# Performance work log

Measured on AMD Instinct MI355X. Metric: run time of the kernel, lower is better.

## Reference

```python
import jax, jax.numpy as jnp
import numpy as np

N_NODES = 100000
N_EDGES = 1600000


def setup_inputs() -> dict:
    key = jax.random.key(0)
    k1, k2, k3, k4 = jax.random.split(key, 4)
    in_c, hid_c, out_c = 128, 128, 64
    x = jax.random.normal(k1, (N_NODES, in_c), dtype=jnp.float32)
    edge_index = jax.random.randint(k2, (2, N_EDGES), 0, N_NODES, dtype=jnp.int64)
    W1 = jax.random.normal(k3, (in_c, hid_c), dtype=jnp.float32) * (1.0 / np.sqrt(in_c))
    b1 = jnp.zeros((hid_c,), dtype=jnp.float32)
    W2 = jax.random.normal(k4, (hid_c, out_c), dtype=jnp.float32) * (1.0 / np.sqrt(hid_c))
    b2 = jnp.zeros((out_c,), dtype=jnp.float32)
    return {"x": x, "edge_index": edge_index, "W1": W1, "b1": b1, "W2": W2, "b2": b2}


def reference(x, edge_index, W1, b1, W2, b2):
    # PyG GCNConv default: add self-loops, symmetric deg normalization, bias.
    N = x.shape[0]
    loops = jnp.arange(N, dtype=edge_index.dtype)
    src = jnp.concatenate([edge_index[0], loops])  # message sources (j)
    dst = jnp.concatenate([edge_index[1], loops])  # aggregation targets (i)
    ones = jnp.ones(src.shape[0], dtype=x.dtype)
    deg = jax.ops.segment_sum(ones, dst, num_segments=N)  # in-degree incl. self-loops
    dis = jnp.where(deg > 0, jax.lax.rsqrt(deg), 0.0)     # deg^{-1/2}, inf->0
    norm = dis[src] * dis[dst]                             # [E+N]

    def gcn(h, W, b):
        h = h @ W                                  # linear transform first (fewer bytes moved)
        msg = h[src] * norm[:, None]               # gather + scale, [E+N, C]
        return jax.ops.segment_sum(msg, dst, num_segments=N) + b

    h = jax.nn.relu(gcn(x, W1, b1))
    return gcn(h, W2, b2)
```

## Files before the change

kernel.cpp:

```cpp
#include <hip/hip_runtime.h>


constexpr int SCAN_CHUNK = 4096;
constexpr int NBKT = 512;
constexpr int EPB  = 8192;
constexpr int CSR_CAP = 12288;

using short8 = __attribute__((ext_vector_type(8))) short;
using f32x4  = __attribute__((ext_vector_type(4))) float;

__device__ __forceinline__ unsigned short f2bf(float f) {
  unsigned u = __float_as_uint(f);
  unsigned r = (u + 0x7FFFu + ((u >> 16) & 1u)) >> 16;
  return (unsigned short)r;
}
__device__ __forceinline__ float bf2f(unsigned short h) {
  return __uint_as_float(((unsigned)h) << 16);
}

__device__ __forceinline__ int ld_idx(const void* ei, int is64, long long i) {
  return is64 ? (int)((const long long*)ei)[i] : ((const int*)ei)[i];
}

__device__ __forceinline__ int sniff64(const unsigned* ei, int tid) {
  unsigned v = (tid < 128) ? ei[2 * tid + 1] : 0u;
  return __syncthreads_or((int)(v != 0u)) ? 0 : 1;
}


__global__ __launch_bounds__(256) void ks_part_g(const int* __restrict__ in,
                                                 int* __restrict__ partial, int m) {
  __shared__ int red[256];
  int b = blockIdx.x, tid = threadIdx.x;
  int base = b * SCAN_CHUNK + tid * 16;
  int s = 0;
#pragma unroll
  for (int i = 0; i < 16; ++i) {
    int idx = base + i;
    if (idx < m) s += in[idx];
  }
  red[tid] = s;
  __syncthreads();
  for (int off = 128; off > 0; off >>= 1) {
    if (tid < off) red[tid] += red[tid + off];
    __syncthreads();
  }
  if (tid == 0) partial[b] = red[0];
}

__global__ __launch_bounds__(256) void k_scan_top(int* __restrict__ partial, int nparts) {
  __shared__ int sums[256];
  int tid = threadIdx.x;
  sums[tid] = (tid < nparts) ? partial[tid] : 0;
  __syncthreads();
  for (int off = 1; off < 256; off <<= 1) {
    int t = (tid >= off) ? sums[tid - off] : 0;
    __syncthreads();
    sums[tid] += t;
    __syncthreads();
  }
  if (tid < nparts) partial[tid] = (tid == 0) ? 0 : sums[tid - 1];
}

__global__ __launch_bounds__(256) void ks_write_g(const int* __restrict__ in,
                                                  const int* __restrict__ partial,
                                                  int* __restrict__ out, int m) {
  __shared__ int tsum[256];
  int b = blockIdx.x, tid = threadIdx.x;
  int base = b * SCAN_CHUNK + tid * 16;
  int vals[16];
  int s = 0;
#pragma unroll
  for (int i = 0; i < 16; ++i) {
    int idx = base + i;
    int v = (idx < m) ? in[idx] : 0;
    vals[i] = s;
    s += v;
  }
  tsum[tid] = s;
  __syncthreads();
  for (int off = 1; off < 256; off <<= 1) {
    int t = (tid >= off) ? tsum[tid - off] : 0;
    __syncthreads();
    tsum[tid] += t;
    __syncthreads();
  }
  int toff = partial[b] + ((tid == 0) ? 0 : tsum[tid - 1]);
#pragma unroll
  for (int i = 0; i < 16; ++i) {
    int idx = base + i;
    if (idx < m) out[idx] = toff + vals[i];
  }
}


__global__ __launch_bounds__(256) void k_hist(const void* __restrict__ ei,
                                              int* __restrict__ hist,
                                              int e, int nblk, int npb) {
  __shared__ int h[NBKT];
  int blk = blockIdx.x, tid = threadIdx.x;
  int is64 = sniff64((const unsigned*)ei, tid);
  for (int i = tid; i < NBKT; i += 256) h[i] = 0;
  __syncthreads();
  int base = blk * EPB;
  int end = base + EPB; if (end > e) end = e;
  for (int i = base + tid; i < end; i += 256) {
    int d = ld_idx(ei, is64, (long long)e + i);
    atomicAdd(&h[d / npb], 1);
  }
  __syncthreads();
  for (int i = tid; i < NBKT; i += 256)
    hist[(size_t)i * nblk + blk] = h[i];
}

__global__ __launch_bounds__(256) void k_partition(const void* __restrict__ ei,
                                                   const int* __restrict__ scanned,
                                                   unsigned* __restrict__ pairbuf,
                                                   int e, int nblk, int npb) {
  __shared__ int off[NBKT];
  int blk = blockIdx.x, tid = threadIdx.x;
  int is64 = sniff64((const unsigned*)ei, tid);
  for (int i = tid; i < NBKT; i += 256)
    off[i] = scanned[(size_t)i * nblk + blk];
  __syncthreads();
  int base = blk * EPB;
  int end = base + EPB; if (end > e) end = e;
  for (int i = base + tid; i < end; i += 256) {
    int s = ld_idx(ei, is64, i);
    int d = ld_idx(ei, is64, (long long)e + i);
    int bkt = d / npb;
    int pos = atomicAdd(&off[bkt], 1);
    pairbuf[pos] = (unsigned)s | ((unsigned)(d - bkt * npb) << 20);
  }
}

__global__ __launch_bounds__(256) void k_bucket_all(const unsigned* __restrict__ pairbuf,
                                                    const int* __restrict__ scanned,
                                                    int* __restrict__ rowptr,
                                                    int* __restrict__ cursor,
                                                    float* __restrict__ dis,
                                                    int* __restrict__ csr,
                                                    int n, int e, int npb, int nblk) {
  __shared__ int lcsr[CSR_CAP];
  __shared__ int cnt[256];
  __shared__ int scn[256];
  int b = blockIdx.x, tid = threadIdx.x;
  if (b == 0 && tid == 0) rowptr[n] = e;
  int lo = b * npb;
  if (lo >= n) return;
  int hi = lo + npb; if (hi > n) hi = n;
  int nn = hi - lo;
  int seg_base = scanned[(size_t)b * nblk];
  int seg_end  = (b == NBKT - 1) ? e : scanned[(size_t)(b + 1) * nblk];
  int cnt_total = seg_end - seg_base;

  for (int i = tid; i < nn; i += 256) cnt[i] = 0;
  __syncthreads();
  for (int i = tid; i < cnt_total; i += 256)
    atomicAdd(&cnt[pairbuf[seg_base + i] >> 20], 1);
  __syncthreads();

  int v = (tid < nn) ? cnt[tid] : 0;
  scn[tid] = v;
  __syncthreads();
  for (int off = 1; off < 256; off <<= 1) {
    int t = (tid >= off) ? scn[tid - off] : 0;
    __syncthreads();
    scn[tid] += t;
    __syncthreads();
  }
  int start = (tid == 0) ? 0 : scn[tid - 1];
  if (tid < nn) {
    int node = lo + tid;
    rowptr[node] = seg_base + start;
    cursor[node] = seg_base + start;
    dis[node] = rsqrtf((float)(v + 1));
  }
  __syncthreads();
  if (tid < nn) cnt[tid] = start;
  __syncthreads();

  if (cnt_total <= CSR_CAP) {
    for (int i = tid; i < cnt_total; i += 256) {
      unsigned p = pairbuf[seg_base + i];
      int q = atomicAdd(&cnt[p >> 20], 1);
      lcsr[q] = (int)(p & 0xFFFFFu);
    }
    __syncthreads();
    for (int i = tid; i < cnt_total; i += 256) csr[seg_base + i] = lcsr[i];
  } else {
    for (int i = tid; i < cnt_total; i += 256) {
      unsigned p = pairbuf[seg_base + i];
      int q = atomicAdd(&cursor[lo + (int)(p >> 20)], 1);
      csr[q] = (int)(p & 0xFFFFFu);
    }
  }
}

template <int NCOL, bool XBF16>
__global__ __launch_bounds__(256) void k_gemm_mfma(const void* __restrict__ Xv,
                                                   const float* __restrict__ W,
                                                   const float* __restrict__ dis,
                                                   unsigned short* __restrict__ S,
                                                   int nrows) {
  constexpr int ROWS = 64;
  constexpr int NCF = NCOL / 16;
  __shared__ __align__(16) unsigned short xs[ROWS * 128];
  __shared__ __align__(16) unsigned short wt[NCOL * 128];
  int tid = threadIdx.x;

  for (int id = tid; id < 128 * NCOL; id += 256) {
    int k = id / NCOL, c = id % NCOL;
    wt[(c * 128 + k) ^ ((c & 7) << 3)] = f2bf(W[id]);
  }

  int wv = tid >> 6, lane = tid & 63;
  int l16 = lane & 15, lk = lane >> 4;
  int arow = wv * 16 + l16;
  int npass = (nrows + ROWS - 1) / ROWS;

  for (int p = blockIdx.x; p < npass; p += gridDim.x) {
    int r0 = p * ROWS;
    __syncthreads();
#pragma unroll
    for (int it = 0; it < 4; ++it) {
      int id = tid + 256 * it;
      int row = id >> 4, kc = id & 15;
      int gr = r0 + row;
      unsigned short v[8];
      if (gr < nrows) {
        if (XBF16) {
          const unsigned short* xb = (const unsigned short*)Xv + (size_t)gr * 128 + kc * 8;
#pragma unroll
          for (int j = 0; j < 8; ++j) v[j] = xb[j];
        } else {
          const float4* x4 = (const float4*)Xv + (size_t)gr * 32 + kc * 2;
          float4 f0 = x4[0], f1 = x4[1];
          v[0] = f2bf(f0.x); v[1] = f2bf(f0.y); v[2] = f2bf(f0.z); v[3] = f2bf(f0.w);
          v[4] = f2bf(f1.x); v[5] = f2bf(f1.y); v[6] = f2bf(f1.z); v[7] = f2bf(f1.w);
        }
      } else {
#pragma unroll
        for (int j = 0; j < 8; ++j) v[j] = 0;
      }
      int idx = (row * 128 + kc * 8) ^ ((row & 7) << 3);
      *(short8*)&xs[idx] = *(short8*)v;
    }
    __syncthreads();

    short8 a[4];
#pragma unroll
    for (int ks = 0; ks < 4; ++ks)
      a[ks] = *(short8*)&xs[(arow * 128 + ks * 32 + lk * 8) ^ ((arow & 7) << 3)];

    f32x4 acc[NCF];
#pragma unroll
    for (int cf = 0; cf < NCF; ++cf) acc[cf] = (f32x4){0.f, 0.f, 0.f, 0.f};

#pragma unroll
    for (int cf = 0; cf < NCF; ++cf) {
      int col = cf * 16 + l16;
#pragma unroll
      for (int ks = 0; ks < 4; ++ks) {
        short8 bfr = *(short8*)&wt[(col * 128 + ks * 32 + lk * 8) ^ ((col & 7) << 3)];
        acc[cf] = __builtin_amdgcn_mfma_f32_16x16x32_bf16(a[ks], bfr, acc[cf], 0, 0, 0);
      }
    }

#pragma unroll
    for (int r = 0; r < 4; ++r) {
      int gr = r0 + wv * 16 + lk * 4 + r;
      if (gr < nrows) {
        float dv = dis[gr];
#pragma unroll
        for (int cf = 0; cf < NCF; ++cf)
          S[(size_t)gr * NCOL + cf * 16 + l16] = f2bf(acc[cf][r] * dv);
      }
    }
  }
}

__global__ __launch_bounds__(256) void k_agg1(const unsigned short* __restrict__ S,
                                              const int* __restrict__ rowptr,
                                              const int* __restrict__ csr,
                                              const float* __restrict__ dis,
                                              const float* __restrict__ b1,
                                              unsigned short* __restrict__ H, int n) {
  int node = blockIdx.x * 4 + (threadIdx.x >> 6);
  if (node >= n) return;
  int lane = threadIdx.x & 63;
  int eg = lane >> 4;
  int cp = lane & 15;
  float acc[8];
  if (eg == 0) {
    short8 v = *(const short8*)&S[(size_t)node * 128 + cp * 8];
#pragma unroll
    for (int k = 0; k < 8; ++k) acc[k] = bf2f((unsigned short)v[k]);
  } else {
#pragma unroll
    for (int k = 0; k < 8; ++k) acc[k] = 0.f;
  }
  int2 rp = *(const int2*)&rowptr[node];
  int e = rp.x + eg;
  for (; e + 12 < rp.y; e += 16) {
    int j0 = csr[e], j1 = csr[e + 4], j2 = csr[e + 8], j3 = csr[e + 12];
    short8 v0 = *(const short8*)&S[(size_t)j0 * 128 + cp * 8];
    short8 v1 = *(const short8*)&S[(size_t)j1 * 128 + cp * 8];
    short8 v2 = *(const short8*)&S[(size_t)j2 * 128 + cp * 8];
    short8 v3 = *(const short8*)&S[(size_t)j3 * 128 + cp * 8];
#pragma unroll
    for (int k = 0; k < 8; ++k)
      acc[k] += (bf2f((unsigned short)v0[k]) + bf2f((unsigned short)v1[k])) +
                (bf2f((unsigned short)v2[k]) + bf2f((unsigned short)v3[k]));
  }
  for (; e < rp.y; e += 4) {
    int j = csr[e];
    short8 v = *(const short8*)&S[(size_t)j * 128 + cp * 8];
#pragma unroll
    for (int k = 0; k < 8; ++k) acc[k] += bf2f((unsigned short)v[k]);
  }
#pragma unroll
  for (int k = 0; k < 8; ++k) {
    acc[k] += __shfl_xor(acc[k], 16);
    acc[k] += __shfl_xor(acc[k], 32);
  }
  if (eg == 0) {
    float d = dis[node];
    float4 bb0 = ((const float4*)b1)[cp * 2];
    float4 bb1 = ((const float4*)b1)[cp * 2 + 1];
    float bv[8] = {bb0.x, bb0.y, bb0.z, bb0.w, bb1.x, bb1.y, bb1.z, bb1.w};
    short8 o;
#pragma unroll
    for (int k = 0; k < 8; ++k)
      o[k] = (short)f2bf(fmaxf(fmaf(acc[k], d, bv[k]), 0.f));
    *(short8*)&H[(size_t)node * 128 + cp * 8] = o;
  }
}

__global__ __launch_bounds__(256) void k_agg2(const unsigned short* __restrict__ S,
                                              const int* __restrict__ rowptr,
                                              const int* __restrict__ csr,
                                              const float* __restrict__ dis,
                                              const float* __restrict__ b2,
                                              float* __restrict__ O, int n) {
  int node = blockIdx.x * 4 + (threadIdx.x >> 6);
  if (node >= n) return;
  int lane = threadIdx.x & 63;
  int eg = lane >> 3;
  int cp = lane & 7;
  float acc[8];
  if (eg == 0) {
    short8 v = *(const short8*)&S[(size_t)node * 64 + cp * 8];
#pragma unroll
    for (int k = 0; k < 8; ++k) acc[k] = bf2f((unsigned short)v[k]);
  } else {
#pragma unroll
    for (int k = 0; k < 8; ++k) acc[k] = 0.f;
  }
  int2 rp = *(const int2*)&rowptr[node];
  int e = rp.x + eg;
  for (; e + 24 < rp.y; e += 32) {
    int j0 = csr[e], j1 = csr[e + 8], j2 = csr[e + 16], j3 = csr[e + 24];
    short8 v0 = *(const short8*)&S[(size_t)j0 * 64 + cp * 8];
    short8 v1 = *(const short8*)&S[(size_t)j1 * 64 + cp * 8];
    short8 v2 = *(const short8*)&S[(size_t)j2 * 64 + cp * 8];
    short8 v3 = *(const short8*)&S[(size_t)j3 * 64 + cp * 8];
#pragma unroll
    for (int k = 0; k < 8; ++k)
      acc[k] += (bf2f((unsigned short)v0[k]) + bf2f((unsigned short)v1[k])) +
                (bf2f((unsigned short)v2[k]) + bf2f((unsigned short)v3[k]));
  }
  for (; e < rp.y; e += 8) {
    int j = csr[e];
    short8 v = *(const short8*)&S[(size_t)j * 64 + cp * 8];
#pragma unroll
    for (int k = 0; k < 8; ++k) acc[k] += bf2f((unsigned short)v[k]);
  }
#pragma unroll
  for (int k = 0; k < 8; ++k) {
    acc[k] += __shfl_xor(acc[k], 8);
    acc[k] += __shfl_xor(acc[k], 16);
    acc[k] += __shfl_xor(acc[k], 32);
  }
  if (eg == 0) {
    float d = dis[node];
    float4 bb0 = ((const float4*)b2)[cp * 2];
    float4 bb1 = ((const float4*)b2)[cp * 2 + 1];
    float bv[8] = {bb0.x, bb0.y, bb0.z, bb0.w, bb1.x, bb1.y, bb1.z, bb1.w};
    float4 o0, o1;
    o0.x = fmaf(acc[0], d, bv[0]); o0.y = fmaf(acc[1], d, bv[1]);
    o0.z = fmaf(acc[2], d, bv[2]); o0.w = fmaf(acc[3], d, bv[3]);
    o1.x = fmaf(acc[4], d, bv[4]); o1.y = fmaf(acc[5], d, bv[5]);
    o1.z = fmaf(acc[6], d, bv[6]); o1.w = fmaf(acc[7], d, bv[7]);
    ((float4*)O)[(size_t)node * 16 + cp * 2] = o0;
    ((float4*)O)[(size_t)node * 16 + cp * 2 + 1] = o1;
  }
}

extern "C" void kernel_launch(void* const* d_in, const int* in_sizes, int n_in,
                              void* d_out, int out_size, void* d_ws, size_t ws_size,
                              hipStream_t stream) {
  const float* x  = (const float*)d_in[0];
  const void*  ei = d_in[1];
  const float* W1 = (const float*)d_in[2];
  const float* b1 = (const float*)d_in[3];
  const float* W2 = (const float*)d_in[4];
  const float* b2 = (const float*)d_in[5];
  float* out = (float*)d_out;

  const int N = in_sizes[0] / 128;
  const int E = in_sizes[1] / 2;
  const int npb  = (N + NBKT - 1) / NBKT;
  const int nblk = (E + EPB - 1) / EPB;
  const int m    = NBKT * nblk;

  char* w = (char*)d_ws;
  size_t off = 0;
  auto alloc = [&](size_t bytes) -> void* {
    void* p = (void*)(w + off);
    off += (bytes + 255) & ~(size_t)255;
    return p;
  };
  int*            rowptr  = (int*)alloc((size_t)(N + 1) * 4);
  int*            cursor  = (int*)alloc((size_t)N * 4);
  float*          dis     = (float*)alloc((size_t)N * 4);
  int*            csr     = (int*)alloc((size_t)E * 4);
  unsigned*       pairbuf = (unsigned*)alloc((size_t)E * 4);
  int*            hist    = (int*)alloc((size_t)m * 4);
  int*            scanned = (int*)alloc((size_t)m * 4);
  unsigned short* s1      = (unsigned short*)alloc((size_t)N * 128 * 2);
  unsigned short* s2      = (unsigned short*)alloc((size_t)N * 64 * 2);
  unsigned short* h       = (unsigned short*)alloc((size_t)N * 128 * 2);
  int*            partial = (int*)alloc(256 * 4);

  int npartsM = (m + SCAN_CHUNK - 1) / SCAN_CHUNK;

  k_hist<<<nblk, 256, 0, stream>>>(ei, hist, E, nblk, npb);
  ks_part_g<<<npartsM, 256, 0, stream>>>(hist, partial, m);
  k_scan_top<<<1, 256, 0, stream>>>(partial, npartsM);
  ks_write_g<<<npartsM, 256, 0, stream>>>(hist, partial, scanned, m);
  k_partition<<<nblk, 256, 0, stream>>>(ei, scanned, pairbuf, E, nblk, npb);
  k_bucket_all<<<NBKT, 256, 0, stream>>>(pairbuf, scanned, rowptr, cursor, dis, csr,
                                         N, E, npb, nblk);

  k_gemm_mfma<128, false><<<1024, 256, 0, stream>>>(x, W1, dis, s1, N);
  k_agg1<<<(N + 3) / 4, 256, 0, stream>>>(s1, rowptr, csr, dis, b1, h, N);
  k_gemm_mfma<64, true><<<1024, 256, 0, stream>>>(h, W2, dis, s2, N);
  k_agg2<<<(N + 3) / 4, 256, 0, stream>>>(s2, rowptr, csr, dis, b2, out, N);
}
```

Baseline: 214.9 us.

## Shrink edges per block, fold top-level scan into write pass, narrow agg unroll

Reduces EPB from 8192 to 2048 so histogram and partition kernels launch more blocks. It removes the separate single-block top-level scan kernel: each write-scan block now sums the preceding partials itself. The aggregation loops unroll by 2 instead of 4, with a single-iteration tail. The tail becomes an if, which only covers the remainder correctly when at most one edge is left per lane group, which holds for the new stride. A smaller EPB also makes m = nblk*NBKT larger, so the scan inputs and the per-block partial prefix loops grow.

Result: faster. 205.1 us (-4.5%).

```diff
diff --git a/kernel.cpp b/kernel.cpp
--- a/kernel.cpp
+++ b/kernel.cpp
@@ -3,7 +3,7 @@
 
 constexpr int SCAN_CHUNK = 4096;
 constexpr int NBKT = 512;
-constexpr int EPB  = 8192;
+constexpr int EPB  = 2048;
 constexpr int CSR_CAP = 12288;
 
 using short8 = __attribute__((ext_vector_type(8))) short;
@@ -48,25 +48,23 @@
   if (tid == 0) partial[b] = red[0];
 }
 
-__global__ __launch_bounds__(256) void k_scan_top(int* __restrict__ partial, int nparts) {
-  __shared__ int sums[256];
-  int tid = threadIdx.x;
-  sums[tid] = (tid < nparts) ? partial[tid] : 0;
-  __syncthreads();
-  for (int off = 1; off < 256; off <<= 1) {
-    int t = (tid >= off) ? sums[tid - off] : 0;
-    __syncthreads();
-    sums[tid] += t;
-    __syncthreads();
-  }
-  if (tid < nparts) partial[tid] = (tid == 0) ? 0 : sums[tid - 1];
-}
-
 __global__ __launch_bounds__(256) void ks_write_g(const int* __restrict__ in,
                                                   const int* __restrict__ partial,
                                                   int* __restrict__ out, int m) {
+  __shared__ int red[256];
   __shared__ int tsum[256];
   int b = blockIdx.x, tid = threadIdx.x;
+  int pb = 0;
+  for (int j = tid; j < b; j += 256) pb += partial[j];
+  red[tid] = pb;
+  __syncthreads();
+  for (int off = 128; off > 0; off >>= 1) {
+    if (tid < off) red[tid] += red[tid + off];
+    __syncthreads();
+  }
+  int block_base = red[0];
+  __syncthreads();
+
   int base = b * SCAN_CHUNK + tid * 16;
   int vals[16];
   int s = 0;
@@ -85,7 +83,7 @@
     tsum[tid] += t;
     __syncthreads();
   }
-  int toff = partial[b] + ((tid == 0) ? 0 : tsum[tid - 1]);
+  int toff = block_base + ((tid == 0) ? 0 : tsum[tid - 1]);
 #pragma unroll
   for (int i = 0; i < 16; ++i) {
     int idx = base + i;
@@ -302,18 +300,15 @@
   }
   int2 rp = *(const int2*)&rowptr[node];
   int e = rp.x + eg;
-  for (; e + 12 < rp.y; e += 16) {
-    int j0 = csr[e], j1 = csr[e + 4], j2 = csr[e + 8], j3 = csr[e + 12];
+  for (; e + 4 < rp.y; e += 8) {
+    int j0 = csr[e], j1 = csr[e + 4];
     short8 v0 = *(const short8*)&S[(size_t)j0 * 128 + cp * 8];
     short8 v1 = *(const short8*)&S[(size_t)j1 * 128 + cp * 8];
-    short8 v2 = *(const short8*)&S[(size_t)j2 * 128 + cp * 8];
-    short8 v3 = *(const short8*)&S[(size_t)j3 * 128 + cp * 8];
 #pragma unroll
     for (int k = 0; k < 8; ++k)
-      acc[k] += (bf2f((unsigned short)v0[k]) + bf2f((unsigned short)v1[k])) +
-                (bf2f((unsigned short)v2[k]) + bf2f((unsigned short)v3[k]));
-  }
-  for (; e < rp.y; e += 4) {
+      acc[k] += bf2f((unsigned short)v0[k]) + bf2f((unsigned short)v1[k]);
+  }
+  if (e < rp.y) {
     int j = csr[e];
     short8 v = *(const short8*)&S[(size_t)j * 128 + cp * 8];
 #pragma unroll
@@ -359,18 +354,15 @@
   }
   int2 rp = *(const int2*)&rowptr[node];
   int e = rp.x + eg;
-  for (; e + 24 < rp.y; e += 32) {
-    int j0 = csr[e], j1 = csr[e + 8], j2 = csr[e + 16], j3 = csr[e + 24];
+  for (; e + 8 < rp.y; e += 16) {
+    int j0 = csr[e], j1 = csr[e + 8];
     short8 v0 = *(const short8*)&S[(size_t)j0 * 64 + cp * 8];
     short8 v1 = *(const short8*)&S[(size_t)j1 * 64 + cp * 8];
-    short8 v2 = *(const short8*)&S[(size_t)j2 * 64 + cp * 8];
-    short8 v3 = *(const short8*)&S[(size_t)j3 * 64 + cp * 8];
 #pragma unroll
     for (int k = 0; k < 8; ++k)
-      acc[k] += (bf2f((unsigned short)v0[k]) + bf2f((unsigned short)v1[k])) +
-                (bf2f((unsigned short)v2[k]) + bf2f((unsigned short)v3[k]));
-  }
-  for (; e < rp.y; e += 8) {
+      acc[k] += bf2f((unsigned short)v0[k]) + bf2f((unsigned short)v1[k]);
+  }
+  if (e < rp.y) {
     int j = csr[e];
     short8 v = *(const short8*)&S[(size_t)j * 64 + cp * 8];
 #pragma unroll
@@ -437,7 +429,6 @@
 
   k_hist<<<nblk, 256, 0, stream>>>(ei, hist, E, nblk, npb);
   ks_part_g<<<npartsM, 256, 0, stream>>>(hist, partial, m);
-  k_scan_top<<<1, 256, 0, stream>>>(partial, npartsM);
   ks_write_g<<<npartsM, 256, 0, stream>>>(hist, partial, scanned, m);
   k_partition<<<nblk, 256, 0, stream>>>(ei, scanned, pairbuf, E, nblk, npb);
   k_bucket_all<<<NBKT, 256, 0, stream>>>(pairbuf, scanned, rowptr, cursor, dis, csr,
```
